# Kernel optimization log

Measured on AMD Instinct MI355X. Metric: run time of the kernel, lower is better.

## Reference

```python
import jax, jax.numpy as jnp
import numpy as np

N = 20000
E = 320000
IN_DIM = 128
HIDDEN = 256
HEADS = 4
HD = HIDDEN // HEADS  # 64 per-head channels in layer 1
OUT_DIM = 128
NEG_SLOPE = 0.2
BN_EPS = 1e-5


def setup_inputs() -> dict:
    key = jax.random.key(0)
    ks = jax.random.split(key, 16)
    inp = {
        "x": jax.random.normal(ks[0], (N, IN_DIM), dtype=jnp.float32),
        "edge_index": jax.random.randint(ks[1], (2, E), 0, N, dtype=jnp.int64),
        # layer 1: GATConv(IN_DIM, HD, heads=HEADS, concat=True)
        "W1": jax.random.normal(ks[2], (IN_DIM, HEADS * HD), dtype=jnp.float32) * (1.0 / np.sqrt(IN_DIM)),
        "att_src1": jax.random.normal(ks[3], (HEADS, HD), dtype=jnp.float32) * 0.1,
        "att_dst1": jax.random.normal(ks[4], (HEADS, HD), dtype=jnp.float32) * 0.1,
        "bias1": jnp.zeros((HEADS * HD,), dtype=jnp.float32),
        "bn1_gamma": jnp.ones((HIDDEN,), dtype=jnp.float32),
        "bn1_beta": jnp.zeros((HIDDEN,), dtype=jnp.float32),
        # layer 2: GATConv(HIDDEN, OUT_DIM, heads=1, concat=False)
        "W2": jax.random.normal(ks[5], (HIDDEN, OUT_DIM), dtype=jnp.float32) * (1.0 / np.sqrt(HIDDEN)),
        "att_src2": jax.random.normal(ks[6], (1, OUT_DIM), dtype=jnp.float32) * 0.1,
        "att_dst2": jax.random.normal(ks[7], (1, OUT_DIM), dtype=jnp.float32) * 0.1,
        "bias2": jnp.zeros((OUT_DIM,), dtype=jnp.float32),
        "bn2_gamma": jnp.ones((OUT_DIM,), dtype=jnp.float32),
        "bn2_beta": jnp.zeros((OUT_DIM,), dtype=jnp.float32),
    }
    return inp


def _gat_conv(x, src, dst, W, a_src, a_dst, bias, heads, concat):
    """PyG GATConv with add_self_loops=True (self-loops already in src/dst)."""
    n = x.shape[0]
    hd = W.shape[1] // heads
    h = (x @ W).reshape(n, heads, hd)                     # [N, H, hd]
    alpha_s = jnp.einsum('nhd,hd->nh', h, a_src)          # [N, H]
    alpha_d = jnp.einsum('nhd,hd->nh', h, a_dst)          # [N, H]
    e = alpha_s[src] + alpha_d[dst]                       # [Etot, H]
    e = jnp.where(e > 0, e, NEG_SLOPE * e)                # leaky_relu
    # edge-softmax over incoming edges of each destination node
    m = jax.ops.segment_max(e, dst, num_segments=n)       # [N, H]
    ex = jnp.exp(e - m[dst])
    denom = jax.ops.segment_sum(ex, dst, num_segments=n)  # [N, H]
    alpha = ex / (denom[dst] + 1e-16)                     # [Etot, H]
    msg = h[src] * alpha[..., None]                       # [Etot, H, hd]
    out = jax.ops.segment_sum(msg, dst, num_segments=n)   # [N, H, hd]
    if concat:
        out = out.reshape(n, heads * hd)
    else:
        out = out.mean(axis=1)
    return out + bias


def _batch_norm(x, gamma, beta):
    mean = x.mean(axis=0)
    var = ((x - mean) ** 2).mean(axis=0)  # biased, training-mode BN
    return (x - mean) * jax.lax.rsqrt(var + BN_EPS) * gamma + beta


def reference(x, edge_index, W1, att_src1, att_dst1, bias1, bn1_gamma, bn1_beta,
              W2, att_src2, att_dst2, bias2, bn2_gamma, bn2_beta):
    n = x.shape[0]
    loop = jnp.arange(n, dtype=edge_index.dtype)
    src = jnp.concatenate([edge_index[0], loop])  # add self-loops (PyG default)
    dst = jnp.concatenate([edge_index[1], loop])

    h = _gat_conv(x, src, dst, W1, att_src1, att_dst1, bias1, HEADS, True)
    h = _batch_norm(h, bn1_gamma, bn1_beta)
    h = jax.nn.elu(h)

    h = _gat_conv(h, src, dst, W2, att_src2, att_dst2, bias2, 1, False)
    h = _batch_norm(h, bn2_gamma, bn2_beta)
    return h
```

## Files before the change

### kernel.cpp

```cpp
#include <hip/hip_runtime.h>
#include <type_traits>

constexpr int N_N  = 20000;
constexpr int N_E  = 320000;
constexpr int N_ET = N_E + N_N;
constexpr int IN_D = 128;
constexpr int HID  = 256;
constexpr int H1   = 4;
constexpr int OUTD = 128;
constexpr float SLOPE = 0.2f;
constexpr float BNEPS = 1e-5f;
constexpr int NPART = 32;

typedef unsigned short u16;
typedef float f32x4 __attribute__((ext_vector_type(4)));
typedef short bf16x8 __attribute__((ext_vector_type(8)));
typedef unsigned short u16x8 __attribute__((ext_vector_type(8)));

__device__ __forceinline__ float bf2f(u16 u) { return __uint_as_float((unsigned)u << 16); }
__device__ __forceinline__ u16 f2bf(float f) {
  unsigned u = __float_as_uint(f);
  unsigned r = u + 0x7FFFu + ((u >> 16) & 1u);
  return (u16)(r >> 16);
}

__global__ __launch_bounds__(256) void prep_k(const int* __restrict__ ei,
                                              const float* __restrict__ W1,
                                              const float* __restrict__ W2,
                                              u16* __restrict__ wp1,
                                              u16* __restrict__ wp2,
                                              int* __restrict__ cnt) {
  const int i = blockIdx.x * 256 + threadIdx.x;
  if (i < IN_D * HID) {
    const int n = i >> 7, k = i & 127;
    wp1[i] = f2bf(W1[(size_t)k * HID + n]);
  }
  if (i < HID * OUTD) {
    const int n = i >> 8, k = i & 255;
    wp2[i] = f2bf(W2[(size_t)k * OUTD + n]);
  }
  if (i < N_ET) {
    const int dst = (i < N_E) ? ei[N_E + i] : (i - N_E);
    atomicAdd(&cnt[dst], 1);
  }
}

__global__ __launch_bounds__(1024) void scan_k(const int* __restrict__ cnt,
                                               int* __restrict__ rowptr,
                                               int* __restrict__ wcur) {
  __shared__ int wsum[17];
  const int tid = threadIdx.x, lane = tid & 63, wv = tid >> 6;
  constexpr int CHK = 20;
  const int base = tid * CHK;
  int c[CHK];
  int s = 0;
#pragma unroll
  for (int j = 0; j < CHK; ++j) {
    const int idx = base + j;
    c[j] = (idx < N_N) ? cnt[idx] : 0;
    s += c[j];
  }
  const int own = s;
#pragma unroll
  for (int off = 1; off < 64; off <<= 1) {
    const int v = __shfl_up(s, off, 64);
    if (lane >= off) s += v;
  }
  if (lane == 63) wsum[wv] = s;
  __syncthreads();
  if (tid == 0) {
    int run = 0;
#pragma unroll
    for (int i = 0; i < 16; ++i) { const int t = wsum[i]; wsum[i] = run; run += t; }
    wsum[16] = run;
  }
  __syncthreads();
  int run = wsum[wv] + (s - own);
#pragma unroll
  for (int j = 0; j < CHK; ++j) {
    const int idx = base + j;
    if (idx < N_N) {
      rowptr[idx] = run;
      wcur[idx]   = run;
      run += c[j];
    }
  }
  if (tid == 0) rowptr[N_N] = wsum[16];
}

constexpr int GB1 = N_N / 16;
__global__ __launch_bounds__(256) void sg_k(const float* __restrict__ x,
                                            const u16* __restrict__ wp,
                                            const float* __restrict__ asrc,
                                            const float* __restrict__ adst,
                                            u16* __restrict__ h,
                                            float* __restrict__ as_,
                                            float* __restrict__ ad_,
                                            const int* __restrict__ ei,
                                            int* __restrict__ wcur,
                                            int* __restrict__ col) {
  const int tid = threadIdx.x;
  if (blockIdx.x >= GB1) {
    const int i = (blockIdx.x - GB1) * 256 + tid;
    if (i >= N_ET) return;
    int s, dst;
    if (i < N_E) { s = ei[i]; dst = ei[N_E + i]; } else { s = dst = i - N_E; }
    const int pos = atomicAdd(&wcur[dst], 1);
    col[pos] = s;
    return;
  }
  const int wv = tid >> 6, lane = tid & 63;
  const int q = lane >> 4, t = lane & 15;
  const int m0 = blockIdx.x * 16;
  const int n0 = wv * 64;
  f32x4 acc[4] = {};
#pragma unroll
  for (int kb = 0; kb < 4; ++kb) {
    const int k0 = kb * 32 + q * 8;
    const float4 x0 = *(const float4*)(x + (size_t)(m0 + t) * 128 + k0);
    const float4 x1 = *(const float4*)(x + (size_t)(m0 + t) * 128 + k0 + 4);
    bf16x8 a;
    a[0] = (short)f2bf(x0.x); a[1] = (short)f2bf(x0.y);
    a[2] = (short)f2bf(x0.z); a[3] = (short)f2bf(x0.w);
    a[4] = (short)f2bf(x1.x); a[5] = (short)f2bf(x1.y);
    a[6] = (short)f2bf(x1.z); a[7] = (short)f2bf(x1.w);
#pragma unroll
    for (int nt = 0; nt < 4; ++nt) {
      const int n = n0 + nt * 16 + t;
      const bf16x8 b = *(const bf16x8*)(wp + (size_t)n * 128 + k0);
      acc[nt] = __builtin_amdgcn_mfma_f32_16x16x32_bf16(a, b, acc[nt], 0, 0, 0);
    }
  }
  float ps[4] = {0.f, 0.f, 0.f, 0.f}, pd[4] = {0.f, 0.f, 0.f, 0.f};
#pragma unroll
  for (int nt = 0; nt < 4; ++nt) {
    const int coln = n0 + nt * 16 + t;
    const float a_s = asrc[coln], a_d = adst[coln];
#pragma unroll
    for (int r = 0; r < 4; ++r) {
      const float d = acc[nt][r];
      h[(size_t)(m0 + q * 4 + r) * 256 + coln] = f2bf(d);
      ps[r] += d * a_s;
      pd[r] += d * a_d;
    }
  }
#pragma unroll
  for (int off = 1; off < 16; off <<= 1)
#pragma unroll
    for (int r = 0; r < 4; ++r) {
      ps[r] += __shfl_xor(ps[r], off, 64);
      pd[r] += __shfl_xor(pd[r], off, 64);
    }
  if (t == 0) {
#pragma unroll
    for (int r = 0; r < 4; ++r) {
      const int row = m0 + q * 4 + r;
      as_[(size_t)row * 4 + wv] = ps[r];
      ad_[(size_t)row * 4 + wv] = pd[r];
    }
  }
}

__global__ __launch_bounds__(256) void gat_agg1_k(const int* __restrict__ rowptr,
                                                  const int* __restrict__ col,
                                                  const u16* __restrict__ h,
                                                  const float* __restrict__ as_,
                                                  const float* __restrict__ ad_,
                                                  u16* __restrict__ out,
                                                  float* __restrict__ accp) {
  __shared__ __align__(16) float s_w[4][64][4];
  __shared__ __align__(16) float st_s[4][256], st_q[4][256];
  const int tid = threadIdx.x;
  const int wv = tid >> 6, lane = tid & 63;
  const int n = blockIdx.x * 4 + wv;
  const int beg = rowptr[n], end = rowptr[n + 1];
  const int eh = lane >> 5;
  const int cp = lane & 31;
  const int c0 = cp * 8;
  const int hl = cp >> 3;
  const float4 adv = *(const float4*)(ad_ + (size_t)n * 4);

  float a[8] = {};
  float smh = 0.f;

  for (int j0 = beg; j0 < end; j0 += 64) {
    const int cnt = min(64, end - j0);
    const int j = j0 + lane;
    const int sl = col[(j < end) ? j : beg];

    u16x8 gA[4];
#pragma unroll
    for (int u = 0; u < 4; ++u) {
      const int sv = __shfl(sl, 2 * u + eh, 64);
      gA[u] = *(const u16x8*)(h + (size_t)sv * 256 + c0);
    }

    const float4 av = *(const float4*)(as_ + (size_t)sl * 4);
    float e0 = av.x + adv.x; e0 = e0 > 0.f ? e0 : SLOPE * e0;
    float e1 = av.y + adv.y; e1 = e1 > 0.f ? e1 : SLOPE * e1;
    float e2 = av.z + adv.z; e2 = e2 > 0.f ? e2 : SLOPE * e2;
    float e3 = av.w + adv.w; e3 = e3 > 0.f ? e3 : SLOPE * e3;
    const bool valid = j < end;
    float4 w4;
    w4.x = valid ? __expf(e0) : 0.f;
    w4.y = valid ? __expf(e1) : 0.f;
    w4.z = valid ? __expf(e2) : 0.f;
    w4.w = valid ? __expf(e3) : 0.f;
    *(float4*)(&s_w[wv][lane][0]) = w4;

    const int rounds = (cnt + 7) >> 3;
    for (int r = 0; r < rounds; ++r) {
      u16x8 gB[4];
      if (r + 1 < rounds) {
        const int nb = (r + 1) * 8;
#pragma unroll
        for (int u = 0; u < 4; ++u) {
          const int sv = __shfl(sl, nb + 2 * u + eh, 64);
          gB[u] = *(const u16x8*)(h + (size_t)sv * 256 + c0);
        }
      }
      const int rb = r * 8;
#pragma unroll
      for (int u = 0; u < 4; ++u) {
        const float w = s_w[wv][rb + 2 * u + eh][hl];
        smh += w;
#pragma unroll
        for (int k = 0; k < 8; ++k) a[k] = fmaf(w, bf2f(gA[u][k]), a[k]);
      }
      if (r + 1 < rounds) {
#pragma unroll
        for (int u = 0; u < 4; ++u) gA[u] = gB[u];
      }
    }
  }

  smh += __shfl_xor(smh, 32, 64);
#pragma unroll
  for (int k = 0; k < 8; ++k) a[k] += __shfl_xor(a[k], 32, 64);

  const float rr = 1.f / (smh + 1e-16f);
  float v[8];
#pragma unroll
  for (int k = 0; k < 8; ++k) v[k] = a[k] * rr;

  if (lane < 32) {
    u16x8 o;
#pragma unroll
    for (int k = 0; k < 8; ++k) o[k] = f2bf(v[k]);
    *(u16x8*)(out + (size_t)n * 256 + c0) = o;
    float4 s0, s1, q0, q1;
    s0.x = v[0]; s0.y = v[1]; s0.z = v[2]; s0.w = v[3];
    s1.x = v[4]; s1.y = v[5]; s1.z = v[6]; s1.w = v[7];
    q0.x = v[0]*v[0]; q0.y = v[1]*v[1]; q0.z = v[2]*v[2]; q0.w = v[3]*v[3];
    q1.x = v[4]*v[4]; q1.y = v[5]*v[5]; q1.z = v[6]*v[6]; q1.w = v[7]*v[7];
    *(float4*)(&st_s[wv][c0])     = s0;
    *(float4*)(&st_s[wv][c0 + 4]) = s1;
    *(float4*)(&st_q[wv][c0])     = q0;
    *(float4*)(&st_q[wv][c0 + 4]) = q1;
  }
  __syncthreads();
  {
    const int c = tid;
    const float s = st_s[0][c] + st_s[1][c] + st_s[2][c] + st_s[3][c];
    const float q = st_q[0][c] + st_q[1][c] + st_q[2][c] + st_q[3][c];
    float* dst = accp + (size_t)(blockIdx.x & (NPART - 1)) * 512;
    atomicAdd(&dst[c], s);
    atomicAdd(&dst[256 + c], q);
  }
}

__global__ __launch_bounds__(256) void gat_agg2_k(const int* __restrict__ rowptr,
                                                  const int* __restrict__ col,
                                                  const u16* __restrict__ h,
                                                  const float* __restrict__ as_,
                                                  const float* __restrict__ ad_,
                                                  u16* __restrict__ out,
                                                  float* __restrict__ accp) {
  __shared__ __align__(16) float st_s[4][128], st_q[4][128];
  const int tid = threadIdx.x;
  const int wv = tid >> 6, lane = tid & 63;
  const int n = blockIdx.x * 4 + wv;
  const int beg = rowptr[n], end = rowptr[n + 1];
  const int eh = lane >> 4;
  const int cp = lane & 15;
  const int c0 = cp * 8;
  const float adv = ad_[n];

  float a[8] = {};
  float smh = 0.f;

  for (int j0 = beg; j0 < end; j0 += 64) {
    const int cnt = min(64, end - j0);
    const int j = j0 + lane;
    const int sl = col[(j < end) ? j : beg];
    float e = as_[sl] + adv;
    e = e > 0.f ? e : SLOPE * e;
    const float ew = (j < end) ? __expf(e) : 0.f;

    const int rounds = (cnt + 15) >> 4;
    u16x8 gA[4];
#pragma unroll
    for (int u = 0; u < 4; ++u) {
      const int sv = __shfl(sl, 4 * u + eh, 64);
      gA[u] = *(const u16x8*)(h + (size_t)sv * 128 + c0);
    }
    for (int r = 0; r < rounds; ++r) {
      u16x8 gB[4];
      if (r + 1 < rounds) {
        const int nb = (r + 1) * 16;
#pragma unroll
        for (int u = 0; u < 4; ++u) {
          const int sv = __shfl(sl, nb + 4 * u + eh, 64);
          gB[u] = *(const u16x8*)(h + (size_t)sv * 128 + c0);
        }
      }
      const int rb = r * 16;
#pragma unroll
      for (int u = 0; u < 4; ++u) {
        const float w = __shfl(ew, rb + 4 * u + eh, 64);
        smh += w;
#pragma unroll
        for (int k = 0; k < 8; ++k) a[k] = fmaf(w, bf2f(gA[u][k]), a[k]);
      }
      if (r + 1 < rounds) {
#pragma unroll
        for (int u = 0; u < 4; ++u) gA[u] = gB[u];
      }
    }
  }

  smh += __shfl_xor(smh, 16, 64);
  smh += __shfl_xor(smh, 32, 64);
#pragma unroll
  for (int k = 0; k < 8; ++k) {
    a[k] += __shfl_xor(a[k], 16, 64);
    a[k] += __shfl_xor(a[k], 32, 64);
  }

  const float rr = 1.f / (smh + 1e-16f);
  float v[8];
#pragma unroll
  for (int k = 0; k < 8; ++k) v[k] = a[k] * rr;

  if (lane < 16) {
    u16x8 o;
#pragma unroll
    for (int k = 0; k < 8; ++k) o[k] = f2bf(v[k]);
    *(u16x8*)(out + (size_t)n * 128 + c0) = o;
    float4 s0, s1, q0, q1;
    s0.x = v[0]; s0.y = v[1]; s0.z = v[2]; s0.w = v[3];
    s1.x = v[4]; s1.y = v[5]; s1.z = v[6]; s1.w = v[7];
    q0.x = v[0]*v[0]; q0.y = v[1]*v[1]; q0.z = v[2]*v[2]; q0.w = v[3]*v[3];
    q1.x = v[4]*v[4]; q1.y = v[5]*v[5]; q1.z = v[6]*v[6]; q1.w = v[7]*v[7];
    *(float4*)(&st_s[wv][c0])     = s0;
    *(float4*)(&st_s[wv][c0 + 4]) = s1;
    *(float4*)(&st_q[wv][c0])     = q0;
    *(float4*)(&st_q[wv][c0 + 4]) = q1;
  }
  __syncthreads();
  if (tid < 128) {
    const int c = tid;
    const float s = st_s[0][c] + st_s[1][c] + st_s[2][c] + st_s[3][c];
    const float q = st_q[0][c] + st_q[1][c] + st_q[2][c] + st_q[3][c];
    float* dst = accp + (size_t)(blockIdx.x & (NPART - 1)) * 256;
    atomicAdd(&dst[c], s);
    atomicAdd(&dst[128 + c], q);
  }
}

__global__ __launch_bounds__(256) void gemm2_mfma_k(const u16* __restrict__ hin,
                                                    const float* __restrict__ accp,
                                                    const float* __restrict__ g1,
                                                    const float* __restrict__ b1,
                                                    const u16* __restrict__ wp,
                                                    const float* __restrict__ asrc,
                                                    const float* __restrict__ adst,
                                                    u16* __restrict__ h2,
                                                    float* __restrict__ as_,
                                                    float* __restrict__ ad_) {
  __shared__ float scsh[512];
  __shared__ float red[2][32][2];
  const int tid = threadIdx.x;
  {
    float s = 0.f, q = 0.f;
#pragma unroll
    for (int p = 0; p < NPART; ++p) {
      s += accp[(size_t)p * 512 + tid];
      q += accp[(size_t)p * 512 + 256 + tid];
    }
    const float mean = s * (1.f / N_N);
    const float var  = q * (1.f / N_N) - mean * mean;
    const float inv  = rsqrtf(var + BNEPS);
    const float sc   = g1[tid] * inv;
    scsh[tid]       = sc;
    scsh[256 + tid] = b1[tid] - mean * sc;
  }
  __syncthreads();
  const int wv = tid >> 6, lane = tid & 63;
  const int q = lane >> 4, t = lane & 15;
  const int mh = wv >> 1, nh = wv & 1;
  const int m0 = blockIdx.x * 32 + mh * 16;
  const int n0 = nh * 64;
  f32x4 acc[4] = {};
#pragma unroll
  for (int kb = 0; kb < 8; ++kb) {
    const int k0 = kb * 32 + q * 8;
    const ushort4 u0 = *(const ushort4*)(hin + (size_t)(m0 + t) * 256 + k0);
    const ushort4 u1 = *(const ushort4*)(hin + (size_t)(m0 + t) * 256 + k0 + 4);
    const float4 sc0 = *(const float4*)(scsh + k0);
    const float4 sc1 = *(const float4*)(scsh + k0 + 4);
    const float4 sh0 = *(const float4*)(scsh + 256 + k0);
    const float4 sh1 = *(const float4*)(scsh + 256 + k0 + 4);
    float v[8];
    v[0] = bf2f(u0.x) * sc0.x + sh0.x;
    v[1] = bf2f(u0.y) * sc0.y + sh0.y;
    v[2] = bf2f(u0.z) * sc0.z + sh0.z;
    v[3] = bf2f(u0.w) * sc0.w + sh0.w;
    v[4] = bf2f(u1.x) * sc1.x + sh1.x;
    v[5] = bf2f(u1.y) * sc1.y + sh1.y;
    v[6] = bf2f(u1.z) * sc1.z + sh1.z;
    v[7] = bf2f(u1.w) * sc1.w + sh1.w;
    bf16x8 a;
#pragma unroll
    for (int j = 0; j < 8; ++j) {
      const float e = v[j] > 0.f ? v[j] : __expf(v[j]) - 1.f;
      a[j] = (short)f2bf(e);
    }
#pragma unroll
    for (int nt = 0; nt < 4; ++nt) {
      const int n = n0 + nt * 16 + t;
      const bf16x8 b = *(const bf16x8*)(wp + (size_t)n * 256 + k0);
      acc[nt] = __builtin_amdgcn_mfma_f32_16x16x32_bf16(a, b, acc[nt], 0, 0, 0);
    }
  }
  float ps[4] = {0.f, 0.f, 0.f, 0.f}, pd[4] = {0.f, 0.f, 0.f, 0.f};
#pragma unroll
  for (int nt = 0; nt < 4; ++nt) {
    const int coln = n0 + nt * 16 + t;
    const float a_s = asrc[coln], a_d = adst[coln];
#pragma unroll
    for (int r = 0; r < 4; ++r) {
      const float d = acc[nt][r];
      h2[(size_t)(m0 + q * 4 + r) * 128 + coln] = f2bf(d);
      ps[r] += d * a_s;
      pd[r] += d * a_d;
    }
  }
#pragma unroll
  for (int off = 1; off < 16; off <<= 1)
#pragma unroll
    for (int r = 0; r < 4; ++r) {
      ps[r] += __shfl_xor(ps[r], off, 64);
      pd[r] += __shfl_xor(pd[r], off, 64);
    }
  if (t == 0) {
#pragma unroll
    for (int r = 0; r < 4; ++r) {
      red[0][mh * 16 + q * 4 + r][nh] = ps[r];
      red[1][mh * 16 + q * 4 + r][nh] = pd[r];
    }
  }
  __syncthreads();
  if (tid < 32) {
    as_[(size_t)blockIdx.x * 32 + tid] = red[0][tid][0] + red[0][tid][1];
    ad_[(size_t)blockIdx.x * 32 + tid] = red[1][tid][0] + red[1][tid][1];
  }
}

__global__ __launch_bounds__(256) void apply_k(const u16* __restrict__ X,
                                               const float* __restrict__ accp,
                                               const float* __restrict__ gamma,
                                               const float* __restrict__ beta,
                                               float* __restrict__ Y) {
  __shared__ float s_sc[128], s_sh[128];
  const int tid = threadIdx.x;
  if (tid < 128) {
    float s = 0.f, q = 0.f;
#pragma unroll
    for (int p = 0; p < NPART; ++p) {
      s += accp[(size_t)p * 256 + tid];
      q += accp[(size_t)p * 256 + 128 + tid];
    }
    const float mean = s * (1.f / N_N);
    const float var  = q * (1.f / N_N) - mean * mean;
    const float inv  = rsqrtf(var + BNEPS);
    const float sc   = gamma[tid] * inv;
    s_sc[tid] = sc;
    s_sh[tid] = beta[tid] - mean * sc;
  }
  __syncthreads();
  constexpr size_t TOT = (size_t)N_N * OUTD;
  for (size_t i = ((size_t)blockIdx.x * 256 + tid) * 4; i < TOT;
       i += (size_t)gridDim.x * 256 * 4) {
    const ushort4 u = *(const ushort4*)(X + i);
    const int c = (int)(i & 127);
    float4 o;
    o.x = bf2f(u.x) * s_sc[c]     + s_sh[c];
    o.y = bf2f(u.y) * s_sc[c + 1] + s_sh[c + 1];
    o.z = bf2f(u.z) * s_sc[c + 2] + s_sh[c + 2];
    o.w = bf2f(u.w) * s_sc[c + 3] + s_sh[c + 3];
    *(float4*)(Y + i) = o;
  }
}

constexpr size_t OFF_WP1  = 0;
constexpr size_t OFF_WP2  = OFF_WP1  + (size_t)IN_D * HID / 2;
constexpr size_t OFF_H1   = OFF_WP2  + (size_t)HID * OUTD / 2;
constexpr size_t OFF_OUT1 = OFF_H1   + (size_t)N_N * HID / 2;
constexpr size_t OFF_H2   = OFF_OUT1 + (size_t)N_N * HID / 2;
constexpr size_t OFF_OUT2 = OFF_H2   + (size_t)N_N * OUTD / 2;
constexpr size_t OFF_AS1  = OFF_OUT2 + (size_t)N_N * OUTD / 2;
constexpr size_t OFF_AD1  = OFF_AS1  + (size_t)N_N * H1;
constexpr size_t OFF_AS2  = OFF_AD1  + (size_t)N_N * H1;
constexpr size_t OFF_AD2  = OFF_AS2  + (size_t)N_N;
constexpr size_t OFF_ROWP = OFF_AD2  + (size_t)N_N;
constexpr size_t OFF_COL  = OFF_ROWP + (size_t)(N_N + 1);
constexpr size_t OFF_WCUR = OFF_COL  + (size_t)N_ET;
constexpr size_t OFF_CNT  = OFF_WCUR + (size_t)N_N;
constexpr size_t OFF_ACC1 = OFF_CNT  + (size_t)N_N;
constexpr size_t OFF_ACC2 = OFF_ACC1 + (size_t)NPART * 512;
constexpr size_t OFF_ZEND = OFF_ACC2 + (size_t)NPART * 256;

extern "C" void kernel_launch(void* const* d_in, const int* in_sizes, int n_in,
                              void* d_out, int out_size, void* d_ws, size_t ws_size,
                              hipStream_t stream) {
  const float* x      = (const float*)d_in[0];
  const int*   ei     = (const int*)d_in[1];
  const float* W1     = (const float*)d_in[2];
  const float* asrc1  = (const float*)d_in[3];
  const float* adst1  = (const float*)d_in[4];
  const float* g1     = (const float*)d_in[6];
  const float* b1     = (const float*)d_in[7];
  const float* W2     = (const float*)d_in[8];
  const float* asrc2  = (const float*)d_in[9];
  const float* adst2  = (const float*)d_in[10];
  const float* g2     = (const float*)d_in[12];
  const float* b2     = (const float*)d_in[13];

  float* ws = (float*)d_ws;
  u16*   wp1   = (u16*)(ws + OFF_WP1);
  u16*   wp2   = (u16*)(ws + OFF_WP2);
  u16*   h1    = (u16*)(ws + OFF_H1);
  u16*   out1  = (u16*)(ws + OFF_OUT1);
  u16*   h2    = (u16*)(ws + OFF_H2);
  u16*   out2  = (u16*)(ws + OFF_OUT2);
  float* as1   = ws + OFF_AS1;
  float* ad1   = ws + OFF_AD1;
  float* as2   = ws + OFF_AS2;
  float* ad2   = ws + OFF_AD2;
  int*   rowp  = (int*)(ws + OFF_ROWP);
  int*   col   = (int*)(ws + OFF_COL);
  int*   wcur  = (int*)(ws + OFF_WCUR);
  int*   cnt   = (int*)(ws + OFF_CNT);
  float* acc1p = ws + OFF_ACC1;
  float* acc2p = ws + OFF_ACC2;
  float* outf  = (float*)d_out;

  hipMemsetAsync(cnt, 0, (OFF_ZEND - OFF_CNT) * sizeof(float), stream);

  const int eb = (N_ET + 255) / 256;
  prep_k<<<eb, 256, 0, stream>>>(ei, W1, W2, wp1, wp2, cnt);
  scan_k<<<1, 1024, 0, stream>>>(cnt, rowp, wcur);
  sg_k<<<GB1 + eb, 256, 0, stream>>>(x, wp1, asrc1, adst1, h1, as1, ad1, ei, wcur, col);
  gat_agg1_k<<<N_N / 4, 256, 0, stream>>>(rowp, col, h1, as1, ad1, out1, acc1p);
  gemm2_mfma_k<<<N_N / 32, 256, 0, stream>>>(out1, acc1p, g1, b1, wp2, asrc2, adst2, h2, as2, ad2);
  gat_agg2_k<<<N_N / 4, 256, 0, stream>>>(rowp, col, h2, as2, ad2, out2, acc2p);
  apply_k<<<512, 256, 0, stream>>>(out2, acc2p, g2, b2, outf);
}
```

Measured before the change: 229.7 us.

## Split GAT aggregation across column slices with one block per slice

Measured after the change: 258.9 us. +12.7%, slower.

```diff
diff --git a/kernel.cpp b/kernel.cpp
--- a/kernel.cpp
+++ b/kernel.cpp
@@ -161,24 +161,26 @@
   }
 }
 
-__global__ __launch_bounds__(256) void gat_agg1_k(const int* __restrict__ rowptr,
-                                                  const int* __restrict__ col,
-                                                  const u16* __restrict__ h,
-                                                  const float* __restrict__ as_,
-                                                  const float* __restrict__ ad_,
-                                                  u16* __restrict__ out,
-                                                  float* __restrict__ accp) {
-  __shared__ __align__(16) float s_w[4][64][4];
-  __shared__ __align__(16) float st_s[4][256], st_q[4][256];
+template<int HSTRIDE, int HEADS, int SLICES>
+__global__ __launch_bounds__(256) void gat_agg_k(const int* __restrict__ rowptr,
+                                                 const int* __restrict__ col,
+                                                 const u16* __restrict__ h,
+                                                 const float* __restrict__ as_,
+                                                 const float* __restrict__ ad_,
+                                                 u16* __restrict__ out,
+                                                 float* __restrict__ accp) {
+  constexpr int LOGS = (SLICES == 4) ? 2 : 1;
+  __shared__ float s_w[4][64];
+  __shared__ __align__(16) float st_s[4][64], st_q[4][64];
   const int tid = threadIdx.x;
   const int wv = tid >> 6, lane = tid & 63;
-  const int n = blockIdx.x * 4 + wv;
+  const int q  = blockIdx.x & (SLICES - 1);
+  const int n  = (blockIdx.x >> LOGS) * 4 + wv;
   const int beg = rowptr[n], end = rowptr[n + 1];
-  const int eh = lane >> 5;
-  const int cp = lane & 31;
-  const int c0 = cp * 8;
-  const int hl = cp >> 3;
-  const float4 adv = *(const float4*)(ad_ + (size_t)n * 4);
+  const int eh = lane >> 3;
+  const int cp = lane & 7;
+  const int c0 = q * 64 + cp * 8;
+  const float adv = ad_[(size_t)n * HEADS + (HEADS == 4 ? q : 0)];
 
   float a[8] = {};
   float smh = 0.f;
@@ -191,38 +193,29 @@
     u16x8 gA[4];
 #pragma unroll
     for (int u = 0; u < 4; ++u) {
-      const int sv = __shfl(sl, 2 * u + eh, 64);
-      gA[u] = *(const u16x8*)(h + (size_t)sv * 256 + c0);
-    }
-
-    const float4 av = *(const float4*)(as_ + (size_t)sl * 4);
-    float e0 = av.x + adv.x; e0 = e0 > 0.f ? e0 : SLOPE * e0;
-    float e1 = av.y + adv.y; e1 = e1 > 0.f ? e1 : SLOPE * e1;
-    float e2 = av.z + adv.z; e2 = e2 > 0.f ? e2 : SLOPE * e2;
-    float e3 = av.w + adv.w; e3 = e3 > 0.f ? e3 : SLOPE * e3;
-    const bool valid = j < end;
-    float4 w4;
-    w4.x = valid ? __expf(e0) : 0.f;
-    w4.y = valid ? __expf(e1) : 0.f;
-    w4.z = valid ? __expf(e2) : 0.f;
-    w4.w = valid ? __expf(e3) : 0.f;
-    *(float4*)(&s_w[wv][lane][0]) = w4;
-
-    const int rounds = (cnt + 7) >> 3;
+      const int sv = __shfl(sl, u * 8 + eh, 64);
+      gA[u] = *(const u16x8*)(h + (size_t)sv * HSTRIDE + c0);
+    }
+
+    float e = as_[(size_t)sl * HEADS + (HEADS == 4 ? q : 0)] + adv;
+    e = e > 0.f ? e : SLOPE * e;
+    s_w[wv][lane] = (j < end) ? __expf(e) : 0.f;
+
+    const int rounds = (cnt + 31) >> 5;
     for (int r = 0; r < rounds; ++r) {
       u16x8 gB[4];
       if (r + 1 < rounds) {
-        const int nb = (r + 1) * 8;
+        const int nb = (r + 1) * 32;
 #pragma unroll
         for (int u = 0; u < 4; ++u) {
-          const int sv = __shfl(sl, nb + 2 * u + eh, 64);
-          gB[u] = *(const u16x8*)(h + (size_t)sv * 256 + c0);
+          const int sv = __shfl(sl, nb + u * 8 + eh, 64);
+          gB[u] = *(const u16x8*)(h + (size_t)sv * HSTRIDE + c0);
         }
       }
-      const int rb = r * 8;
+      const int rb = r * 32;
 #pragma unroll
       for (int u = 0; u < 4; ++u) {
-        const float w = s_w[wv][rb + 2 * u + eh][hl];
+        const float w = s_w[wv][rb + u * 8 + eh];
         smh += w;
 #pragma unroll
         for (int k = 0; k < 8; ++k) a[k] = fmaf(w, bf2f(gA[u][k]), a[k]);
@@ -234,137 +227,45 @@
     }
   }
 
+  smh += __shfl_xor(smh, 8, 64);
+  smh += __shfl_xor(smh, 16, 64);
   smh += __shfl_xor(smh, 32, 64);
 #pragma unroll
-  for (int k = 0; k < 8; ++k) a[k] += __shfl_xor(a[k], 32, 64);
+  for (int k = 0; k < 8; ++k) {
+    a[k] += __shfl_xor(a[k], 8, 64);
+    a[k] += __shfl_xor(a[k], 16, 64);
+    a[k] += __shfl_xor(a[k], 32, 64);
+  }
 
   const float rr = 1.f / (smh + 1e-16f);
   float v[8];
 #pragma unroll
   for (int k = 0; k < 8; ++k) v[k] = a[k] * rr;
 
-  if (lane < 32) {
+  if (lane < 8) {
     u16x8 o;
 #pragma unroll
     for (int k = 0; k < 8; ++k) o[k] = f2bf(v[k]);
-    *(u16x8*)(out + (size_t)n * 256 + c0) = o;
+    *(u16x8*)(out + (size_t)n * HSTRIDE + c0) = o;
     float4 s0, s1, q0, q1;
     s0.x = v[0]; s0.y = v[1]; s0.z = v[2]; s0.w = v[3];
     s1.x = v[4]; s1.y = v[5]; s1.z = v[6]; s1.w = v[7];
     q0.x = v[0]*v[0]; q0.y = v[1]*v[1]; q0.z = v[2]*v[2]; q0.w = v[3]*v[3];
     q1.x = v[4]*v[4]; q1.y = v[5]*v[5]; q1.z = v[6]*v[6]; q1.w = v[7]*v[7];
-    *(float4*)(&st_s[wv][c0])     = s0;
-    *(float4*)(&st_s[wv][c0 + 4]) = s1;
-    *(float4*)(&st_q[wv][c0])     = q0;
-    *(float4*)(&st_q[wv][c0 + 4]) = q1;
-  }
-  __syncthreads();
-  {
+    const int cb = lane * 8;
+    *(float4*)(&st_s[wv][cb])     = s0;
+    *(float4*)(&st_s[wv][cb + 4]) = s1;
+    *(float4*)(&st_q[wv][cb])     = q0;
+    *(float4*)(&st_q[wv][cb + 4]) = q1;
+  }
+  __syncthreads();
+  if (tid < 64) {
     const int c = tid;
-    const float s = st_s[0][c] + st_s[1][c] + st_s[2][c] + st_s[3][c];
-    const float q = st_q[0][c] + st_q[1][c] + st_q[2][c] + st_q[3][c];
-    float* dst = accp + (size_t)(blockIdx.x & (NPART - 1)) * 512;
-    atomicAdd(&dst[c], s);
-    atomicAdd(&dst[256 + c], q);
-  }
-}
-
-__global__ __launch_bounds__(256) void gat_agg2_k(const int* __restrict__ rowptr,
-                                                  const int* __restrict__ col,
-                                                  const u16* __restrict__ h,
-                                                  const float* __restrict__ as_,
-                                                  const float* __restrict__ ad_,
-                                                  u16* __restrict__ out,
-                                                  float* __restrict__ accp) {
-  __shared__ __align__(16) float st_s[4][128], st_q[4][128];
-  const int tid = threadIdx.x;
-  const int wv = tid >> 6, lane = tid & 63;
-  const int n = blockIdx.x * 4 + wv;
-  const int beg = rowptr[n], end = rowptr[n + 1];
-  const int eh = lane >> 4;
-  const int cp = lane & 15;
-  const int c0 = cp * 8;
-  const float adv = ad_[n];
-
-  float a[8] = {};
-  float smh = 0.f;
-
-  for (int j0 = beg; j0 < end; j0 += 64) {
-    const int cnt = min(64, end - j0);
-    const int j = j0 + lane;
-    const int sl = col[(j < end) ? j : beg];
-    float e = as_[sl] + adv;
-    e = e > 0.f ? e : SLOPE * e;
-    const float ew = (j < end) ? __expf(e) : 0.f;
-
-    const int rounds = (cnt + 15) >> 4;
-    u16x8 gA[4];
-#pragma unroll
-    for (int u = 0; u < 4; ++u) {
-      const int sv = __shfl(sl, 4 * u + eh, 64);
-      gA[u] = *(const u16x8*)(h + (size_t)sv * 128 + c0);
-    }
-    for (int r = 0; r < rounds; ++r) {
-      u16x8 gB[4];
-      if (r + 1 < rounds) {
-        const int nb = (r + 1) * 16;
-#pragma unroll
-        for (int u = 0; u < 4; ++u) {
-          const int sv = __shfl(sl, nb + 4 * u + eh, 64);
-          gB[u] = *(const u16x8*)(h + (size_t)sv * 128 + c0);
-        }
-      }
-      const int rb = r * 16;
-#pragma unroll
-      for (int u = 0; u < 4; ++u) {
-        const float w = __shfl(ew, rb + 4 * u + eh, 64);
-        smh += w;
-#pragma unroll
-        for (int k = 0; k < 8; ++k) a[k] = fmaf(w, bf2f(gA[u][k]), a[k]);
-      }
-      if (r + 1 < rounds) {
-#pragma unroll
-        for (int u = 0; u < 4; ++u) gA[u] = gB[u];
-      }
-    }
-  }
-
-  smh += __shfl_xor(smh, 16, 64);
-  smh += __shfl_xor(smh, 32, 64);
-#pragma unroll
-  for (int k = 0; k < 8; ++k) {
-    a[k] += __shfl_xor(a[k], 16, 64);
-    a[k] += __shfl_xor(a[k], 32, 64);
-  }
-
-  const float rr = 1.f / (smh + 1e-16f);
-  float v[8];
-#pragma unroll
-  for (int k = 0; k < 8; ++k) v[k] = a[k] * rr;
-
-  if (lane < 16) {
-    u16x8 o;
-#pragma unroll
-    for (int k = 0; k < 8; ++k) o[k] = f2bf(v[k]);
-    *(u16x8*)(out + (size_t)n * 128 + c0) = o;
-    float4 s0, s1, q0, q1;
-    s0.x = v[0]; s0.y = v[1]; s0.z = v[2]; s0.w = v[3];
-    s1.x = v[4]; s1.y = v[5]; s1.z = v[6]; s1.w = v[7];
-    q0.x = v[0]*v[0]; q0.y = v[1]*v[1]; q0.z = v[2]*v[2]; q0.w = v[3]*v[3];
-    q1.x = v[4]*v[4]; q1.y = v[5]*v[5]; q1.z = v[6]*v[6]; q1.w = v[7]*v[7];
-    *(float4*)(&st_s[wv][c0])     = s0;
-    *(float4*)(&st_s[wv][c0 + 4]) = s1;
-    *(float4*)(&st_q[wv][c0])     = q0;
-    *(float4*)(&st_q[wv][c0 + 4]) = q1;
-  }
-  __syncthreads();
-  if (tid < 128) {
-    const int c = tid;
-    const float s = st_s[0][c] + st_s[1][c] + st_s[2][c] + st_s[3][c];
-    const float q = st_q[0][c] + st_q[1][c] + st_q[2][c] + st_q[3][c];
-    float* dst = accp + (size_t)(blockIdx.x & (NPART - 1)) * 256;
-    atomicAdd(&dst[c], s);
-    atomicAdd(&dst[128 + c], q);
+    const float s  = st_s[0][c] + st_s[1][c] + st_s[2][c] + st_s[3][c];
+    const float qq = st_q[0][c] + st_q[1][c] + st_q[2][c] + st_q[3][c];
+    float* dst = accp + (size_t)(blockIdx.x & (NPART - 1)) * (2 * HSTRIDE);
+    atomicAdd(&dst[q * 64 + c], s);
+    atomicAdd(&dst[HSTRIDE + q * 64 + c], qq);
   }
 }
 
@@ -562,8 +463,8 @@
   prep_k<<<eb, 256, 0, stream>>>(ei, W1, W2, wp1, wp2, cnt);
   scan_k<<<1, 1024, 0, stream>>>(cnt, rowp, wcur);
   sg_k<<<GB1 + eb, 256, 0, stream>>>(x, wp1, asrc1, adst1, h1, as1, ad1, ei, wcur, col);
-  gat_agg1_k<<<N_N / 4, 256, 0, stream>>>(rowp, col, h1, as1, ad1, out1, acc1p);
+  gat_agg_k<HID, H1, 4><<<(N_N / 4) * 4, 256, 0, stream>>>(rowp, col, h1, as1, ad1, out1, acc1p);
   gemm2_mfma_k<<<N_N / 32, 256, 0, stream>>>(out1, acc1p, g1, b1, wp2, asrc2, adst2, h2, as2, ad2);
-  gat_agg2_k<<<N_N / 4, 256, 0, stream>>>(rowp, col, h2, as2, ad2, out2, acc2p);
+  gat_agg_k<OUTD, 1, 2><<<(N_N / 4) * 2, 256, 0, stream>>>(rowp, col, h2, as2, ad2, out2, acc2p);
   apply_k<<<512, 256, 0, stream>>>(out2, acc2p, g2, b2, outf);
 }
```
